# Kernel optimization log

Hardware: AMD Instinct MI355X
Metric: run time of the kernel (lower is better)

The kernel has to match this reference:

```python
import jax, jax.numpy as jnp
import numpy as np

B, T, D, H = 16, 64, 256, 1536  # batch, num_seq (trg_len), input_dim, hid_dim


def setup_inputs() -> dict:
    key = jax.random.key(0)
    ks = jax.random.split(key, 6)
    def w(k, shape, fan):
        return jax.random.normal(k, shape, jnp.float32) / np.sqrt(fan).astype(np.float32)
    return {
        "batch": jax.random.normal(ks[0], (B, T, D), jnp.float32),
        # PyTorch LSTM params, gate order (i, f, g, o), layer 0 and layer 1
        "W_ih0": w(ks[1], (4 * H, D), H),
        "W_hh0": w(ks[2], (4 * H, H), H),
        "b_ih0": jnp.zeros((4 * H,), jnp.float32),
        "b_hh0": jnp.zeros((4 * H,), jnp.float32),
        "W_ih1": w(ks[3], (4 * H, H), H),
        "W_hh1": w(ks[4], (4 * H, H), H),
        "b_ih1": jnp.zeros((4 * H,), jnp.float32),
        "b_hh1": jnp.zeros((4 * H,), jnp.float32),
    }


def _lstm_cell(pre, c):
    # pre: [4H] pre-activation gates in PyTorch order i, f, g, o
    i, f, g, o = jnp.split(pre, 4, axis=-1)
    c_new = jax.nn.sigmoid(f) * c + jax.nn.sigmoid(i) * jnp.tanh(g)
    h_new = jax.nn.sigmoid(o) * jnp.tanh(c_new)
    return h_new, c_new


def reference(batch, W_ih0, W_hh0, b_ih0, b_hh0, W_ih1, W_hh1, b_ih1, b_hh1):
    hdim = W_hh0.shape[1]
    dt = batch.dtype
    # The original loop runs the unbatched 2-layer LSTM over batch[:, ei, :]
    # (length-B sequence) for ei = 1..T-1, carrying state => one scan over a
    # flattened sequence of length (T-1)*B, ordered ei-major, b-minor.
    seq = batch[:, 1:, :].transpose(1, 0, 2).reshape(-1, batch.shape[2])  # [(T-1)*B, D]
    # Precompute layer-0 input projection as one GEMM (dropout=0.3 is between
    # layers in train mode only; reference is eval mode, so no dropout).
    x_pre0 = seq @ W_ih0.T + (b_ih0 + b_hh0)  # [(T-1)*B, 4H]
    b1 = b_ih1 + b_hh1

    def step(carry, xp0):
        h, c = carry  # each [2, H] (num_layers, hid_dim), unbatched
        h0, c0 = _lstm_cell(xp0 + h[0] @ W_hh0.T, c[0])
        h1, c1 = _lstm_cell(h0 @ W_ih1.T + h[1] @ W_hh1.T + b1, c[1])
        return (jnp.stack([h0, h1]), jnp.stack([c0, c1])), None

    init = (jnp.zeros((2, hdim), dt), jnp.zeros((2, hdim), dt))
    (h_final, c_final), _ = jax.lax.scan(step, init, x_pre0)
    return h_final, c_final  # each [2, H], matching (encoder_hidden, encoder_cell)
```

## Files before the change

### kernel.cpp

```cpp
#include <hip/hip_runtime.h>
#include <cstdint>

#define HDIM   1536
#define DIN    256
#define NSTEP  1008
#define NWG    256
#define TPB    512
#define UPW    6
#define XN     256
#define NREP   8

#define C_H0      0
#define C_H1      1024
#define REP_STRIDE 2048
#define WS_FLAG_W 32768

typedef uint32_t u32x4 __attribute__((ext_vector_type(4)));

__device__ __forceinline__ float bflo(uint32_t p){ union{uint32_t u; float f;} v; v.u = p << 16; return v.f; }
__device__ __forceinline__ float bfhi(uint32_t p){ union{uint32_t u; float f;} v; v.u = p & 0xffff0000u; return v.f; }
__device__ __forceinline__ float bf2f(uint16_t b){ union{uint32_t u; float f;} v; v.u = ((uint32_t)b) << 16; return v.f; }
__device__ __forceinline__ uint16_t f2bf(float f){
    union{float f; uint32_t u;} v; v.f = f;
    uint32_t r = v.u + 0x7fffu + ((v.u >> 16) & 1u);
    return (uint16_t)(r >> 16);
}
__device__ __forceinline__ uint32_t packbf(float lo, float hi){
    return (uint32_t)f2bf(lo) | ((uint32_t)f2bf(hi) << 16);
}
__device__ __forceinline__ float tanh_fast(float x){
    return 1.f - 2.f/(__expf(2.f*x) + 1.f);
}

#if __has_builtin(__builtin_amdgcn_fdot2_f32_bf16)
typedef __bf16 bf16x2 __attribute__((ext_vector_type(2)));
__device__ __forceinline__ float dot2bf(uint32_t a, uint32_t b, float c){
    return __builtin_amdgcn_fdot2_f32_bf16(__builtin_bit_cast(bf16x2, a),
                                           __builtin_bit_cast(bf16x2, b), c, false);
}
#else
__device__ __forceinline__ float dot2bf(uint32_t a, uint32_t b, float c){
    c = fmaf(bflo(a), bflo(b), c);
    c = fmaf(bfhi(a), bfhi(b), c);
    return c;
}
#endif

__device__ __forceinline__ u32x4 poll16(const uint64_t* p){
    u32x4 r;
    asm volatile("global_load_dwordx4 %0, %1, off sc0 sc1\n\t"
                 "s_waitcnt vmcnt(0)"
                 : "=v"(r) : "v"(p) : "memory");
    return r;
}

__device__ __forceinline__ float wave_sum(float x){
    #pragma unroll
    for (int o = 1; o < 64; o <<= 1) x += __shfl_xor(x, o, 64);
    return x;
}

__global__ void init_ws(const uint32_t* __restrict__ w, uint32_t* __restrict__ ws){
    uint64_t* ws64 = (uint64_t*)ws;
    const int i = blockIdx.x * blockDim.x + threadIdx.x;
    if (i < NREP*512){
        const int rep = i >> 9, j = i & 511;
        uint64_t* base = ws64 + rep*REP_STRIDE;
        base[C_H0 + 512 + j] = 0ull;
        base[C_H1 + j]       = 0ull;
        base[C_H1 + 512 + j] = ((uint64_t)1 << 48);
    }
    if (blockIdx.x == 0 && threadIdx.x < 64){
        const int t = threadIdx.x;
        int cnt = 0;
        #pragma unroll
        for (int j = 0; j < 4; ++j){
            const uint32_t v = w[t*4 + j];
            const uint32_t e = (v >> 7) & 0xFFu;
            if (e == 0u || (e >= 0x70u && e <= 0x7Cu)) cnt++;
        }
        #pragma unroll
        for (int o = 1; o < 64; o <<= 1) cnt += __shfl_xor(cnt, o, 64);
        if (t == 0)
            ws[WS_FLAG_W] = (cnt < 128) ? 1u : 0u;
    }
}

__global__ __launch_bounds__(TPB, 2)
void lstm_seq_kernel(const void* __restrict__ batch_,
                     const void* __restrict__ Wih0_,
                     const void* __restrict__ Whh0_,
                     const void* __restrict__ bih0_,
                     const void* __restrict__ bhh0_,
                     const void* __restrict__ Wih1_,
                     const void* __restrict__ Whh1_,
                     const void* __restrict__ bih1_,
                     const void* __restrict__ bhh1_,
                     void* __restrict__ out_,
                     uint32_t* __restrict__ ws)
{
    __shared__ uint32_t lds_w[8*3*8*64];
    __shared__ uint32_t lds_h[1536];
    __shared__ float    lds_pre[48];
    __shared__ float    lds_b[48];
    __shared__ float    lds_c[12];
    __shared__ float    lds_hout[12];

    const int g   = blockIdx.x;
    const int tid = threadIdx.x;
    const int w   = tid >> 6;
    const int l   = tid & 63;

    const uint32_t fp32in = __hip_atomic_load(&ws[WS_FLAG_W],
                             __ATOMIC_RELAXED, __HIP_MEMORY_SCOPE_AGENT);
    uint64_t* ws64 = (uint64_t*)ws;

    if (tid < 24){
        const int uu = tid >> 2, gate = tid & 3;
        const int grow = gate*HDIM + g*UPW + uu;
        if (fp32in){
            lds_b[tid]      = ((const float*)bih0_)[grow] + ((const float*)bhh0_)[grow];
            lds_b[24 + tid] = ((const float*)bih1_)[grow] + ((const float*)bhh1_)[grow];
        } else {
            lds_b[tid]      = bf2f(((const uint16_t*)bih0_)[grow]) + bf2f(((const uint16_t*)bhh0_)[grow]);
            lds_b[24 + tid] = bf2f(((const uint16_t*)bih1_)[grow]) + bf2f(((const uint16_t*)bhh1_)[grow]);
        }
    }
    if (tid < 12){ lds_c[tid] = 0.f; lds_hout[tid] = 0.f; }

    uint32_t w0[3][14];
    uint32_t w1r[3][16];

    if (fp32in){
        const float2* Wih0f = (const float2*)Wih0_;
        const float2* Whh0f = (const float2*)Whh0_;
        const float2* Wih1f = (const float2*)Wih1_;
        const float2* Whh1f = (const float2*)Whh1_;
        #pragma unroll
        for (int j = 0; j < 3; ++j){
            const int rr = w*3 + j;
            const int grow = (rr & 3)*HDIM + g*UPW + (rr >> 2);
            float2 t;
            t = Wih0f[grow*(DIN/2) + l];        w0[j][0] = packbf(t.x, t.y);
            t = Wih0f[grow*(DIN/2) + 64 + l];   w0[j][1] = packbf(t.x, t.y);
            #pragma unroll
            for (int c = 2; c < 14; ++c){
                t = Whh0f[grow*(HDIM/2) + (c-2)*64 + l]; w0[j][c] = packbf(t.x, t.y);
            }
            #pragma unroll
            for (int c = 0; c < 8; ++c){
                t = Wih1f[grow*(HDIM/2) + c*64 + l];
                lds_w[((w*3 + j)*8 + c)*64 + l] = packbf(t.x, t.y);
            }
            #pragma unroll
            for (int c = 8; c < 12; ++c){
                t = Wih1f[grow*(HDIM/2) + c*64 + l]; w1r[j][c-8] = packbf(t.x, t.y);
            }
            #pragma unroll
            for (int c = 12; c < 24; ++c){
                t = Whh1f[grow*(HDIM/2) + (c-12)*64 + l]; w1r[j][c-8] = packbf(t.x, t.y);
            }
        }
    } else {
        const uint32_t* Wih0p = (const uint32_t*)Wih0_;
        const uint32_t* Whh0p = (const uint32_t*)Whh0_;
        const uint32_t* Wih1p = (const uint32_t*)Wih1_;
        const uint32_t* Whh1p = (const uint32_t*)Whh1_;
        #pragma unroll
        for (int j = 0; j < 3; ++j){
            const int rr = w*3 + j;
            const int grow = (rr & 3)*HDIM + g*UPW + (rr >> 2);
            w0[j][0] = Wih0p[grow*(DIN/2) + l];
            w0[j][1] = Wih0p[grow*(DIN/2) + 64 + l];
            #pragma unroll
            for (int c = 2; c < 14; ++c)
                w0[j][c] = Whh0p[grow*(HDIM/2) + (c-2)*64 + l];
            #pragma unroll
            for (int c = 0; c < 8; ++c)
                lds_w[((w*3 + j)*8 + c)*64 + l] = Wih1p[grow*(HDIM/2) + c*64 + l];
            #pragma unroll
            for (int c = 8; c < 12; ++c)
                w1r[j][c-8] = Wih1p[grow*(HDIM/2) + c*64 + l];
            #pragma unroll
            for (int c = 12; c < 24; ++c)
                w1r[j][c-8] = Whh1p[grow*(HDIM/2) + (c-12)*64 + l];
        }
    }

    const int players = tid >> 8;
    const int pidx    = tid & 255;
    uint64_t* myrep   = ws64 + (g & (NREP-1))*REP_STRIDE;

    for (int n = 0; n <= NSTEP; ++n){
        uint32_t xp0, xp1;
        {
            const int nn = (n < NSTEP) ? n : 0;
            const int xbase = ((nn & 15)*64 + (nn >> 4) + 1) * XN;
            if (fp32in){
                const float2* bp = (const float2*)((const float*)batch_ + xbase);
                const float2 t0 = bp[l];
                const float2 t1 = bp[64 + l];
                xp0 = packbf(t0.x, t0.y); xp1 = packbf(t1.x, t1.y);
            } else {
                const uint32_t* bp = (const uint32_t*)batch_ + (xbase >> 1);
                xp0 = bp[l]; xp1 = bp[64 + l];
            }
        }

        u32x4 r;
        {
            const uint64_t* ap = myrep
                + (players ? (C_H1 + (n & 1)*512) : (C_H0 + ((n+1) & 1)*512))
                + 2*pidx;
            const uint32_t want = (uint32_t)n & 0xFFFFu;
            r = poll16(ap);
            while ((r.y >> 16) != want || (r.w >> 16) != want){
                __builtin_amdgcn_s_sleep(1);
                r = poll16(ap);
            }
        }
        {
            const int base = players*768 + 3*pidx;
            lds_h[base]     = r.x;
            lds_h[base + 1] = (r.y & 0xFFFFu) | (r.z << 16);
            lds_h[base + 2] = (r.z >> 16)     | (r.w << 16);
        }
        __syncthreads();

        uint32_t h0p[12], h1p[12];
        #pragma unroll
        for (int k = 0; k < 12; ++k) h0p[k] = lds_h[k*64 + l];
        #pragma unroll
        for (int k = 0; k < 12; ++k) h1p[k] = lds_h[768 + k*64 + l];

        float acc0[3], acc1[3];
        #pragma unroll
        for (int j = 0; j < 3; ++j){
            float a = dot2bf(w0[j][0], xp0, 0.f);
            a = dot2bf(w0[j][1], xp1, a);
            #pragma unroll
            for (int k = 0; k < 12; ++k)
                a = dot2bf(w0[j][k+2], h0p[k], a);
            acc0[j] = a;
        }
        #pragma unroll
        for (int j = 0; j < 3; ++j){
            float a = 0.f;
            #pragma unroll
            for (int k = 0; k < 8; ++k)
                a = dot2bf(lds_w[((w*3 + j)*8 + k)*64 + l], h0p[k], a);
            #pragma unroll
            for (int k = 8; k < 12; ++k)
                a = dot2bf(w1r[j][k-8], h0p[k], a);
            #pragma unroll
            for (int k = 0; k < 12; ++k)
                a = dot2bf(w1r[j][k+4], h1p[k], a);
            acc1[j] = a;
        }
        #pragma unroll
        for (int j = 0; j < 3; ++j){
            const float r0 = wave_sum(acc0[j]);
            const float r1 = wave_sum(acc1[j]);
            if (l == 0){
                lds_pre[w*3 + j]      = r0;
                lds_pre[24 + w*3 + j] = r1;
            }
        }
        __syncthreads();

        if (w == 0){
            float hpub = 0.f;
            if (l < 12){
                const int layer = l / 6, uu = l % 6;
                const bool active = (layer == 0) ? (n < NSTEP) : (n >= 1);
                if (active){
                    const float* pre = &lds_pre[layer*24 + uu*4];
                    const float* bb  = &lds_b[layer*24 + uu*4];
                    const float gi = pre[0] + bb[0];
                    const float gf = pre[1] + bb[1];
                    const float gg = pre[2] + bb[2];
                    const float go = pre[3] + bb[3];
                    const float si = 1.f/(1.f + __expf(-gi));
                    const float sf = 1.f/(1.f + __expf(-gf));
                    const float so = 1.f/(1.f + __expf(-go));
                    const float cn = sf*lds_c[l] + si*tanh_fast(gg);
                    const float hn = so * tanh_fast(cn);
                    lds_c[l] = cn;
                    lds_hout[l] = hn;
                    hpub = hn;
                }
            }
            const int slot = l & 3;
            const int b3 = 3*slot;
            const float s0 = __shfl(hpub, b3,     64);
            const float s1 = __shfl(hpub, b3 + 1, 64);
            const float s2 = __shfl(hpub, b3 + 2, 64);
            if (l < 4*NREP && n < NSTEP){
                const bool isL1 = (slot >= 2);
                if (!isL1 || n >= 1){
                    const uint64_t tag = (uint64_t)((uint32_t)(n + 1) & 0xFFFFu);
                    const uint64_t pk = (uint64_t)f2bf(s0)
                                      | ((uint64_t)f2bf(s1) << 16)
                                      | ((uint64_t)f2bf(s2) << 32)
                                      | (tag << 48);
                    uint64_t* dst = ws64 + (l >> 2)*REP_STRIDE
                        + (isL1 ? (C_H1 + ((n+1) & 1)*512 + 2*g + (slot - 2))
                                : (C_H0 + (n & 1)*512 + 2*g + slot));
                    __hip_atomic_store(dst, pk, __ATOMIC_RELAXED, __HIP_MEMORY_SCOPE_AGENT);
                }
            }
        }
    }

    if (tid < 12){
        const int layer = tid / 6, uu = tid % 6;
        const int oi = layer*HDIM + g*UPW + uu;
        if (fp32in){
            ((float*)out_)[oi]        = lds_hout[tid];
            ((float*)out_)[3072 + oi] = lds_c[tid];
        } else {
            ((uint16_t*)out_)[oi]        = f2bf(lds_hout[tid]);
            ((uint16_t*)out_)[3072 + oi] = f2bf(lds_c[tid]);
        }
    }
}

extern "C" void kernel_launch(void* const* d_in, const int* in_sizes, int n_in,
                              void* d_out, int out_size, void* d_ws, size_t ws_size,
                              hipStream_t stream)
{
    (void)in_sizes; (void)n_in; (void)out_size; (void)ws_size;
    const void* batch = d_in[0];
    const void* Wih0  = d_in[1];
    const void* Whh0  = d_in[2];
    const void* bih0  = d_in[3];
    const void* bhh0  = d_in[4];
    const void* Wih1  = d_in[5];
    const void* Whh1  = d_in[6];
    const void* bih1  = d_in[7];
    const void* bhh1  = d_in[8];
    void* out = d_out;
    uint32_t* ws = (uint32_t*)d_ws;

    hipLaunchKernelGGL(init_ws, dim3((NREP*512 + 255)/256), dim3(256), 0, stream,
                       (const uint32_t*)Whh0, ws);

    void* args[] = { &batch, &Wih0, &Whh0, &bih0, &bhh0,
                     &Wih1, &Whh1, &bih1, &bhh1, &out, &ws };
    hipLaunchCooperativeKernel((const void*)lstm_seq_kernel,
                               dim3(NWG), dim3(TPB), args, 0, stream);
}
```

Measured before the change: 3.506 ms.

## Publish layer-0 hidden state before computing layer-1 gates each step

```diff
diff --git a/kernel.cpp b/kernel.cpp
--- a/kernel.cpp
+++ b/kernel.cpp
@@ -227,13 +227,11 @@
         }
         __syncthreads();
 
-        uint32_t h0p[12], h1p[12];
+        uint32_t h0p[12];
         #pragma unroll
         for (int k = 0; k < 12; ++k) h0p[k] = lds_h[k*64 + l];
-        #pragma unroll
-        for (int k = 0; k < 12; ++k) h1p[k] = lds_h[768 + k*64 + l];
-
-        float acc0[3], acc1[3];
+
+        float acc0[3];
         #pragma unroll
         for (int j = 0; j < 3; ++j){
             float a = dot2bf(w0[j][0], xp0, 0.f);
@@ -245,6 +243,52 @@
         }
         #pragma unroll
         for (int j = 0; j < 3; ++j){
+            const float r0 = wave_sum(acc0[j]);
+            if (l == 0) lds_pre[w*3 + j] = r0;
+        }
+        __syncthreads();
+
+        if (w == 0){
+            float hpub = 0.f;
+            if (l < 6 && n < NSTEP){
+                const float* pre = &lds_pre[l*4];
+                const float* bb  = &lds_b[l*4];
+                const float gi = pre[0] + bb[0];
+                const float gf = pre[1] + bb[1];
+                const float gg = pre[2] + bb[2];
+                const float go = pre[3] + bb[3];
+                const float si = 1.f/(1.f + __expf(-gi));
+                const float sf = 1.f/(1.f + __expf(-gf));
+                const float so = 1.f/(1.f + __expf(-go));
+                const float cn = sf*lds_c[l] + si*tanh_fast(gg);
+                const float hn = so * tanh_fast(cn);
+                lds_c[l] = cn;
+                lds_hout[l] = hn;
+                hpub = hn;
+            }
+            const int slot = l & 1;
+            const float s0 = __shfl(hpub, 3*slot,     64);
+            const float s1 = __shfl(hpub, 3*slot + 1, 64);
+            const float s2 = __shfl(hpub, 3*slot + 2, 64);
+            if (l < 2*NREP && n < NSTEP){
+                const uint64_t tag = (uint64_t)((uint32_t)(n + 1) & 0xFFFFu);
+                const uint64_t pk = (uint64_t)f2bf(s0)
+                                  | ((uint64_t)f2bf(s1) << 16)
+                                  | ((uint64_t)f2bf(s2) << 32)
+                                  | (tag << 48);
+                uint64_t* dst = ws64 + (l >> 1)*REP_STRIDE
+                              + C_H0 + (n & 1)*512 + 2*g + slot;
+                __hip_atomic_store(dst, pk, __ATOMIC_RELAXED, __HIP_MEMORY_SCOPE_AGENT);
+            }
+        }
+
+        uint32_t h1p[12];
+        #pragma unroll
+        for (int k = 0; k < 12; ++k) h1p[k] = lds_h[768 + k*64 + l];
+
+        float acc1[3];
+        #pragma unroll
+        for (int j = 0; j < 3; ++j){
             float a = 0.f;
             #pragma unroll
             for (int k = 0; k < 8; ++k)
@@ -259,59 +303,47 @@
         }
         #pragma unroll
         for (int j = 0; j < 3; ++j){
-            const float r0 = wave_sum(acc0[j]);
             const float r1 = wave_sum(acc1[j]);
-            if (l == 0){
-                lds_pre[w*3 + j]      = r0;
-                lds_pre[24 + w*3 + j] = r1;
-            }
+            if (l == 0) lds_pre[24 + w*3 + j] = r1;
         }
         __syncthreads();
 
-        if (w == 0){
+        if (w == 1){
             float hpub = 0.f;
-            if (l < 12){
-                const int layer = l / 6, uu = l % 6;
-                const bool active = (layer == 0) ? (n < NSTEP) : (n >= 1);
-                if (active){
-                    const float* pre = &lds_pre[layer*24 + uu*4];
-                    const float* bb  = &lds_b[layer*24 + uu*4];
-                    const float gi = pre[0] + bb[0];
-                    const float gf = pre[1] + bb[1];
-                    const float gg = pre[2] + bb[2];
-                    const float go = pre[3] + bb[3];
-                    const float si = 1.f/(1.f + __expf(-gi));
-                    const float sf = 1.f/(1.f + __expf(-gf));
-                    const float so = 1.f/(1.f + __expf(-go));
-                    const float cn = sf*lds_c[l] + si*tanh_fast(gg);
-                    const float hn = so * tanh_fast(cn);
-                    lds_c[l] = cn;
-                    lds_hout[l] = hn;
-                    hpub = hn;
-                }
-            }
-            const int slot = l & 3;
-            const int b3 = 3*slot;
-            const float s0 = __shfl(hpub, b3,     64);
-            const float s1 = __shfl(hpub, b3 + 1, 64);
-            const float s2 = __shfl(hpub, b3 + 2, 64);
-            if (l < 4*NREP && n < NSTEP){
-                const bool isL1 = (slot >= 2);
-                if (!isL1 || n >= 1){
-                    const uint64_t tag = (uint64_t)((uint32_t)(n + 1) & 0xFFFFu);
-                    const uint64_t pk = (uint64_t)f2bf(s0)
-                                      | ((uint64_t)f2bf(s1) << 16)
-                                      | ((uint64_t)f2bf(s2) << 32)
-                                      | (tag << 48);
-                    uint64_t* dst = ws64 + (l >> 2)*REP_STRIDE
-                        + (isL1 ? (C_H1 + ((n+1) & 1)*512 + 2*g + (slot - 2))
-                                : (C_H0 + (n & 1)*512 + 2*g + slot));
-                    __hip_atomic_store(dst, pk, __ATOMIC_RELAXED, __HIP_MEMORY_SCOPE_AGENT);
-                }
-            }
-        }
-    }
-
+            if (l < 6 && n >= 1){
+                const float* pre = &lds_pre[24 + l*4];
+                const float* bb  = &lds_b[24 + l*4];
+                const float gi = pre[0] + bb[0];
+                const float gf = pre[1] + bb[1];
+                const float gg = pre[2] + bb[2];
+                const float go = pre[3] + bb[3];
+                const float si = 1.f/(1.f + __expf(-gi));
+                const float sf = 1.f/(1.f + __expf(-gf));
+                const float so = 1.f/(1.f + __expf(-go));
+                const float cn = sf*lds_c[6 + l] + si*tanh_fast(gg);
+                const float hn = so * tanh_fast(cn);
+                lds_c[6 + l] = cn;
+                lds_hout[6 + l] = hn;
+                hpub = hn;
+            }
+            const int slot = l & 1;
+            const float s0 = __shfl(hpub, 3*slot,     64);
+            const float s1 = __shfl(hpub, 3*slot + 1, 64);
+            const float s2 = __shfl(hpub, 3*slot + 2, 64);
+            if (l < 2*NREP && n >= 1 && n < NSTEP){
+                const uint64_t tag = (uint64_t)((uint32_t)(n + 1) & 0xFFFFu);
+                const uint64_t pk = (uint64_t)f2bf(s0)
+                                  | ((uint64_t)f2bf(s1) << 16)
+                                  | ((uint64_t)f2bf(s2) << 32)
+                                  | (tag << 48);
+                uint64_t* dst = ws64 + (l >> 1)*REP_STRIDE
+                              + C_H1 + ((n+1) & 1)*512 + 2*g + slot;
+                __hip_atomic_store(dst, pk, __ATOMIC_RELAXED, __HIP_MEMORY_SCOPE_AGENT);
+            }
+        }
+    }
+
+    __syncthreads();
     if (tid < 12){
         const int layer = tid / 6, uu = tid % 6;
         const int oi = layer*HDIM + g*UPW + uu;
```

New measurement: 3.783 ms. 7.9% more time.
